# Performance work log

Measured on AMD Instinct MI355X. Metric: run time of the kernel, lower is better.

The kernel has to match this reference:

```python
import jax, jax.numpy as jnp
import numpy as np

N, E = 50000, 800000
IN_DIM, OUT_DIM, REL_DIM = 128, 64, 32
NEG_SLOPE = 0.01  # torch F.leaky_relu default


def setup_inputs() -> dict:
    key = jax.random.key(0)
    ks = jax.random.split(key, 12)
    return {
        "h": jax.random.normal(ks[0], (N, IN_DIM), jnp.float32),
        "relation": jax.random.normal(ks[1], (E, REL_DIM), jnp.float32),
        "score": jax.random.normal(ks[2], (E, 1), jnp.float32),
        "timestamp": jax.random.normal(ks[3], (E, 1), jnp.float32),
        "src": jax.random.randint(ks[4], (E,), 0, N, jnp.int32),
        "dst": jax.random.randint(ks[5], (E,), 0, N, jnp.int32),
        "W_n": jax.random.normal(ks[6], (IN_DIM, OUT_DIM), jnp.float32) / np.sqrt(IN_DIM),
        "W_r": jax.random.normal(ks[7], (REL_DIM, OUT_DIM), jnp.float32) / np.sqrt(REL_DIM),
        "W_s": jax.random.normal(ks[8], (1, OUT_DIM), jnp.float32),
        "W_t": jax.random.normal(ks[9], (1, OUT_DIM), jnp.float32),
        "a": jax.random.normal(ks[10], (5 * OUT_DIM,), jnp.float32) / np.sqrt(5 * OUT_DIM),
    }


def reference(h, relation, score, timestamp, src, dst, W_n, W_r, W_s, W_t, a):
    D = W_n.shape[1]
    z = h @ W_n                     # (N, D)
    er = relation @ W_r             # (E, D)
    es = score @ W_s                # (E, D)
    et = timestamp @ W_t            # (E, D)
    z_src = z[src]                  # (E, D) gather
    z_dst = z[dst]                  # (E, D) gather
    # attn_fc on concat([z_src, z_dst, er, es, et]) == sum of slice dot-products
    a1, a2, a3, a4, a5 = (a[0:D], a[D:2*D], a[2*D:3*D], a[3*D:4*D], a[4*D:5*D])
    logit = z_src @ a1 + z_dst @ a2 + er @ a3 + es @ a4 + et @ a5  # (E,)
    logit = jnp.where(logit >= 0, logit, NEG_SLOPE * logit)        # leaky_relu
    # segment softmax over edges grouped by dst node
    n = z.shape[0]
    seg_max = jax.ops.segment_max(logit, dst, num_segments=n)     # (N,)
    ex = jnp.exp(logit - seg_max[dst])                             # (E,)
    seg_sum = jax.ops.segment_sum(ex, dst, num_segments=n)        # (N,)
    alpha = ex / seg_sum[dst]                                      # (E,)
    # weighted scatter-sum of source features to dst nodes
    h_out = jax.ops.segment_sum(alpha[:, None] * z_src, dst, num_segments=n)  # (N, D)
    return h_out
```

## Files before the change

### kernel.cpp

```cpp
#include <hip/hip_runtime.h>

#define IN_DIM 128
#define OUT_DIM 64
#define REL_DIM 32
#define NEG_SLOPE 0.01f
#define CAP 64

__global__ void k_consts(const float* __restrict__ W_r, const float* __restrict__ W_s,
                         const float* __restrict__ W_t, const float* __restrict__ a,
                         float* __restrict__ consts ) {
    int t = threadIdx.x;
    if (t < REL_DIM) {
        const float* a3 = a + 2 * OUT_DIM;
        float acc = 0.f;
        for (int d = 0; d < OUT_DIM; ++d) acc += W_r[t * OUT_DIM + d] * a3[d];
        consts[t] = acc;
    } else if (t == 32) {
        float acc = 0.f;
        for (int d = 0; d < OUT_DIM; ++d) acc += W_s[d] * a[3 * OUT_DIM + d];
        consts[32] = acc;
    } else if (t == 33) {
        float acc = 0.f;
        for (int d = 0; d < OUT_DIM; ++d) acc += W_t[d] * a[4 * OUT_DIM + d];
        consts[33] = acc;
    }
}

__global__ __launch_bounds__(256) void k_node(const float* __restrict__ h,
                                              const float* __restrict__ W_n,
                                              const float* __restrict__ a,
                                              float* __restrict__ z,
                                              float* __restrict__ s1,
                                              float* __restrict__ s2, int n) {
    __shared__ float hs[IN_DIM * 65];
    __shared__ float s1p[4][64], s2p[4][64];
    int base = blockIdx.x * 64;

    for (int i = threadIdx.x; i < 64 * 32; i += 256) {
        int r = i >> 5;
        int c4 = i & 31;
        float4 v = make_float4(0.f, 0.f, 0.f, 0.f);
        if (base + r < n) v = ((const float4*)(h + (size_t)(base + r) * IN_DIM))[c4];
        int k0 = c4 * 4;
        hs[(k0 + 0) * 65 + r] = v.x;
        hs[(k0 + 1) * 65 + r] = v.y;
        hs[(k0 + 2) * 65 + r] = v.z;
        hs[(k0 + 3) * 65 + r] = v.w;
    }
    __syncthreads();

    int lane = threadIdx.x & 63;
    int w = __builtin_amdgcn_readfirstlane(threadIdx.x >> 6);
    int c0 = w * 16;
    int row = base + lane;

    float acc[16];
    #pragma unroll
    for (int j = 0; j < 16; ++j) acc[j] = 0.f;

    const float* __restrict__ Wslice = W_n + c0;
    #pragma unroll 4
    for (int k = 0; k < IN_DIM; ++k) {
        float hv = hs[k * 65 + lane];
        const float* __restrict__ Wr = Wslice + k * OUT_DIM;
        #pragma unroll
        for (int j = 0; j < 16; ++j) acc[j] = fmaf(hv, Wr[j], acc[j]);
    }

    float p1 = 0.f, p2 = 0.f;
    #pragma unroll
    for (int j = 0; j < 16; ++j) {
        p1 = fmaf(acc[j], a[c0 + j], p1);
        p2 = fmaf(acc[j], a[OUT_DIM + c0 + j], p2);
    }
    s1p[w][lane] = p1;
    s2p[w][lane] = p2;

    if (row < n) {
        float4* zp = (float4*)(z + (size_t)row * OUT_DIM + c0);
        zp[0] = make_float4(acc[0], acc[1], acc[2], acc[3]);
        zp[1] = make_float4(acc[4], acc[5], acc[6], acc[7]);
        zp[2] = make_float4(acc[8], acc[9], acc[10], acc[11]);
        zp[3] = make_float4(acc[12], acc[13], acc[14], acc[15]);
    }
    __syncthreads();
    if (threadIdx.x < 64 && base + (int)threadIdx.x < n) {
        int l = threadIdx.x;
        s1[base + l] = s1p[0][l] + s1p[1][l] + s1p[2][l] + s1p[3][l];
        s2[base + l] = s2p[0][l] + s2p[1][l] + s2p[2][l] + s2p[3][l];
    }
}

__global__ __launch_bounds__(256) void k_fill(const float* __restrict__ rel,
                                              const float* __restrict__ score,
                                              const float* __restrict__ ts,
                                              const int* __restrict__ src,
                                              const int* __restrict__ dst,
                                              const float* __restrict__ s1,
                                              const float* __restrict__ s2,
                                              const float* __restrict__ consts,
                                              int* __restrict__ cnt,
                                              int2* __restrict__ pedge, int E) {
    int tid = blockIdx.x * 256 + threadIdx.x;
    int e = tid >> 3;
    int sub = tid & 7;
    if (e >= E) return;

    float4 w = ((const float4*)consts)[sub];
    float4 v = ((const float4*)rel)[(size_t)e * 8 + sub];
    float dot = v.x * w.x + v.y * w.y + v.z * w.z + v.w * w.w;
    dot += __shfl_xor(dot, 1, 8);
    dot += __shfl_xor(dot, 2, 8);
    dot += __shfl_xor(dot, 4, 8);

    if (sub == 0) {
        int s = src[e], d = dst[e];
        float lg = dot + s1[s] + s2[d] + score[e] * consts[32] + ts[e] * consts[33];
        lg = (lg >= 0.f) ? lg : NEG_SLOPE * lg;
        int rank = atomicAdd(cnt + d, 1);
        if (rank < CAP)
            pedge[((size_t)d << 6) + rank] = make_int2(s, __float_as_int(lg));
    }
}

__global__ __launch_bounds__(256) void k_out(const int* __restrict__ cnt,
                                             const int2* __restrict__ pedge,
                                             const float* __restrict__ z,
                                             float* __restrict__ out, int n) {
    int lane = threadIdx.x & 63;
    int wave = (blockIdx.x * blockDim.x + threadIdx.x) >> 6;
    int nwaves = (gridDim.x * blockDim.x) >> 6;
    int eg = lane >> 4;
    int dl = lane & 15;
    for (int node = wave; node < n; node += nwaves) {
        int deg = min(cnt[node], CAP);
        float4 acc = make_float4(0.f, 0.f, 0.f, 0.f);
        if (deg > 0) {
            int2 pe = make_int2(0, (int)0xff800000u);
            if (lane < deg) pe = pedge[((size_t)node << 6) + lane];
            float v = __int_as_float(pe.y);
            float m = v;
            #pragma unroll
            for (int o = 32; o > 0; o >>= 1) m = fmaxf(m, __shfl_xor(m, o, 64));
            float ex = __expf(v - m);
            float ssum = ex;
            #pragma unroll
            for (int o = 32; o > 0; o >>= 1) ssum += __shfl_xor(ssum, o, 64);
            float alpha = ex * (1.0f / ssum);
            for (int j0 = 0; j0 < deg; j0 += 4) {
                int j = j0 + eg;
                int jc = (j < 64) ? j : 63;
                float wj = __shfl(alpha, jc, 64);
                int  sj = __shfl(pe.x, jc, 64);
                if (j < deg) {
                    float4 zv = ((const float4*)(z + (size_t)sj * OUT_DIM))[dl];
                    acc.x = fmaf(wj, zv.x, acc.x);
                    acc.y = fmaf(wj, zv.y, acc.y);
                    acc.z = fmaf(wj, zv.z, acc.z);
                    acc.w = fmaf(wj, zv.w, acc.w);
                }
            }
        }
        #pragma unroll
        for (int o = 16; o <= 32; o <<= 1) {
            acc.x += __shfl_xor(acc.x, o, 64);
            acc.y += __shfl_xor(acc.y, o, 64);
            acc.z += __shfl_xor(acc.z, o, 64);
            acc.w += __shfl_xor(acc.w, o, 64);
        }
        if (eg == 0) ((float4*)(out + (size_t)node * OUT_DIM))[dl] = acc;
    }
}

extern "C" void kernel_launch(void* const* d_in, const int* in_sizes, int n_in,
                              void* d_out, int out_size, void* d_ws, size_t ws_size,
                              hipStream_t stream) {
    const float* h         = (const float*)d_in[0];
    const float* relation  = (const float*)d_in[1];
    const float* score     = (const float*)d_in[2];
    const float* timestamp = (const float*)d_in[3];
    const int*   src       = (const int*)d_in[4];
    const int*   dst       = (const int*)d_in[5];
    const float* W_n       = (const float*)d_in[6];
    const float* W_r       = (const float*)d_in[7];
    const float* W_s       = (const float*)d_in[8];
    const float* W_t       = (const float*)d_in[9];
    const float* a         = (const float*)d_in[10];

    int n = in_sizes[0] / IN_DIM;
    int E = in_sizes[4];

    float* ws      = (float*)d_ws;
    float* z       = ws;
    float* s1      = z + (size_t)n * OUT_DIM;
    float* s2      = s1 + n;
    float* consts  = s2 + n;
    int*   cnt     = (int*)(consts + 64);
    int2*  pedge   = (int2*)(cnt + n);

    float* out = (float*)d_out;

    hipMemsetAsync(cnt, 0, (size_t)n * sizeof(int), stream);

    k_consts<<<1, 64, 0, stream>>>(W_r, W_s, W_t, a, consts);
    k_node<<<(n + 63) / 64, 256, 0, stream>>>(h, W_n, a, z, s1, s2, n);
    int nfb = (int)(((long long)E * 8 + 255) / 256);
    k_fill<<<nfb, 256, 0, stream>>>(relation, score, timestamp, src, dst,
                                    s1, s2, consts, cnt, pedge, E);
    k_out<<<(n + 3) / 4, 256, 0, stream>>>(cnt, pedge, z, out, n);
}
```

Baseline: 282.0 us.

## Fold memset and constants into kernels, stage W_n in LDS, pair nodes in k_out

The separate memset and k_consts launches are removed. Counter zeroing moves into k_node, and every k_fill block recomputes the relation, score and timestamp attention constants into shared memory. k_node now stages W_n in LDS in two halves instead of reading it from global memory inside the inner loop. k_out handles two destination nodes per wave to expose more independent gathers. The trade-offs are redundant constant computation in every k_fill block, an extra barrier there, and higher LDS use in k_node, which may lower occupancy.

```diff
diff --git a/kernel.cpp b/kernel.cpp
--- a/kernel.cpp
+++ b/kernel.cpp
@@ -6,35 +6,20 @@
 #define NEG_SLOPE 0.01f
 #define CAP 64
 
-__global__ void k_consts(const float* __restrict__ W_r, const float* __restrict__ W_s,
-                         const float* __restrict__ W_t, const float* __restrict__ a,
-                         float* __restrict__ consts ) {
-    int t = threadIdx.x;
-    if (t < REL_DIM) {
-        const float* a3 = a + 2 * OUT_DIM;
-        float acc = 0.f;
-        for (int d = 0; d < OUT_DIM; ++d) acc += W_r[t * OUT_DIM + d] * a3[d];
-        consts[t] = acc;
-    } else if (t == 32) {
-        float acc = 0.f;
-        for (int d = 0; d < OUT_DIM; ++d) acc += W_s[d] * a[3 * OUT_DIM + d];
-        consts[32] = acc;
-    } else if (t == 33) {
-        float acc = 0.f;
-        for (int d = 0; d < OUT_DIM; ++d) acc += W_t[d] * a[4 * OUT_DIM + d];
-        consts[33] = acc;
-    }
-}
-
 __global__ __launch_bounds__(256) void k_node(const float* __restrict__ h,
                                               const float* __restrict__ W_n,
                                               const float* __restrict__ a,
                                               float* __restrict__ z,
                                               float* __restrict__ s1,
-                                              float* __restrict__ s2, int n) {
+                                              float* __restrict__ s2,
+                                              int* __restrict__ cnt, int n) {
     __shared__ float hs[IN_DIM * 65];
+    __shared__ float Wl[64 * OUT_DIM];
     __shared__ float s1p[4][64], s2p[4][64];
     int base = blockIdx.x * 64;
+
+    int gi = blockIdx.x * 256 + threadIdx.x;
+    if (gi < n) cnt[gi] = 0;
 
     for (int i = threadIdx.x; i < 64 * 32; i += 256) {
         int r = i >> 5;
@@ -47,7 +32,6 @@
         hs[(k0 + 2) * 65 + r] = v.z;
         hs[(k0 + 3) * 65 + r] = v.w;
     }
-    __syncthreads();
 
     int lane = threadIdx.x & 63;
     int w = __builtin_amdgcn_readfirstlane(threadIdx.x >> 6);
@@ -58,13 +42,33 @@
     #pragma unroll
     for (int j = 0; j < 16; ++j) acc[j] = 0.f;
 
-    const float* __restrict__ Wslice = W_n + c0;
-    #pragma unroll 4
-    for (int k = 0; k < IN_DIM; ++k) {
-        float hv = hs[k * 65 + lane];
-        const float* __restrict__ Wr = Wslice + k * OUT_DIM;
-        #pragma unroll
-        for (int j = 0; j < 16; ++j) acc[j] = fmaf(hv, Wr[j], acc[j]);
+    for (int kh = 0; kh < 2; ++kh) {
+        __syncthreads();
+        for (int i = threadIdx.x; i < 64 * OUT_DIM / 4; i += 256)
+            ((float4*)Wl)[i] = ((const float4*)(W_n + (size_t)kh * 64 * OUT_DIM))[i];
+        __syncthreads();
+        #pragma unroll 4
+        for (int kk = 0; kk < 64; ++kk) {
+            float hv = hs[(kh * 64 + kk) * 65 + lane];
+            const float4* Wk = (const float4*)(Wl + kk * OUT_DIM + c0);
+            float4 w0 = Wk[0], w1 = Wk[1], w2 = Wk[2], w3 = Wk[3];
+            acc[0]  = fmaf(hv, w0.x, acc[0]);
+            acc[1]  = fmaf(hv, w0.y, acc[1]);
+            acc[2]  = fmaf(hv, w0.z, acc[2]);
+            acc[3]  = fmaf(hv, w0.w, acc[3]);
+            acc[4]  = fmaf(hv, w1.x, acc[4]);
+            acc[5]  = fmaf(hv, w1.y, acc[5]);
+            acc[6]  = fmaf(hv, w1.z, acc[6]);
+            acc[7]  = fmaf(hv, w1.w, acc[7]);
+            acc[8]  = fmaf(hv, w2.x, acc[8]);
+            acc[9]  = fmaf(hv, w2.y, acc[9]);
+            acc[10] = fmaf(hv, w2.z, acc[10]);
+            acc[11] = fmaf(hv, w2.w, acc[11]);
+            acc[12] = fmaf(hv, w3.x, acc[12]);
+            acc[13] = fmaf(hv, w3.y, acc[13]);
+            acc[14] = fmaf(hv, w3.z, acc[14]);
+            acc[15] = fmaf(hv, w3.w, acc[15]);
+        }
     }
 
     float p1 = 0.f, p2 = 0.f;
@@ -98,24 +102,47 @@
                                               const int* __restrict__ dst,
                                               const float* __restrict__ s1,
                                               const float* __restrict__ s2,
-                                              const float* __restrict__ consts,
+                                              const float* __restrict__ W_r,
+                                              const float* __restrict__ W_s,
+                                              const float* __restrict__ W_t,
+                                              const float* __restrict__ a,
                                               int* __restrict__ cnt,
                                               int2* __restrict__ pedge, int E) {
-    int tid = blockIdx.x * 256 + threadIdx.x;
+    __shared__ __align__(16) float cw[36];
+    int t = threadIdx.x;
+    if (t < REL_DIM) {
+        const float* a3 = a + 2 * OUT_DIM;
+        float acc = 0.f;
+        #pragma unroll
+        for (int d2 = 0; d2 < OUT_DIM; ++d2)
+            acc = fmaf(W_r[t * OUT_DIM + d2], a3[d2], acc);
+        cw[t] = acc;
+    } else if (t == 32) {
+        float acc = 0.f;
+        for (int d2 = 0; d2 < OUT_DIM; ++d2) acc = fmaf(W_s[d2], a[3 * OUT_DIM + d2], acc);
+        cw[32] = acc;
+    } else if (t == 33) {
+        float acc = 0.f;
+        for (int d2 = 0; d2 < OUT_DIM; ++d2) acc = fmaf(W_t[d2], a[4 * OUT_DIM + d2], acc);
+        cw[33] = acc;
+    }
+    __syncthreads();
+
+    int tid = blockIdx.x * 256 + t;
     int e = tid >> 3;
     int sub = tid & 7;
     if (e >= E) return;
 
-    float4 w = ((const float4*)consts)[sub];
+    float4 w4 = ((const float4*)cw)[sub];
     float4 v = ((const float4*)rel)[(size_t)e * 8 + sub];
-    float dot = v.x * w.x + v.y * w.y + v.z * w.z + v.w * w.w;
+    float dot = v.x * w4.x + v.y * w4.y + v.z * w4.z + v.w * w4.w;
     dot += __shfl_xor(dot, 1, 8);
     dot += __shfl_xor(dot, 2, 8);
     dot += __shfl_xor(dot, 4, 8);
 
     if (sub == 0) {
         int s = src[e], d = dst[e];
-        float lg = dot + s1[s] + s2[d] + score[e] * consts[32] + ts[e] * consts[33];
+        float lg = dot + s1[s] + s2[d] + score[e] * cw[32] + ts[e] * cw[33];
         lg = (lg >= 0.f) ? lg : NEG_SLOPE * lg;
         int rank = atomicAdd(cnt + d, 1);
         if (rank < CAP)
@@ -132,43 +159,73 @@
     int nwaves = (gridDim.x * blockDim.x) >> 6;
     int eg = lane >> 4;
     int dl = lane & 15;
-    for (int node = wave; node < n; node += nwaves) {
-        int deg = min(cnt[node], CAP);
-        float4 acc = make_float4(0.f, 0.f, 0.f, 0.f);
-        if (deg > 0) {
-            int2 pe = make_int2(0, (int)0xff800000u);
-            if (lane < deg) pe = pedge[((size_t)node << 6) + lane];
-            float v = __int_as_float(pe.y);
-            float m = v;
-            #pragma unroll
-            for (int o = 32; o > 0; o >>= 1) m = fmaxf(m, __shfl_xor(m, o, 64));
-            float ex = __expf(v - m);
-            float ssum = ex;
-            #pragma unroll
-            for (int o = 32; o > 0; o >>= 1) ssum += __shfl_xor(ssum, o, 64);
-            float alpha = ex * (1.0f / ssum);
-            for (int j0 = 0; j0 < deg; j0 += 4) {
-                int j = j0 + eg;
-                int jc = (j < 64) ? j : 63;
-                float wj = __shfl(alpha, jc, 64);
-                int  sj = __shfl(pe.x, jc, 64);
-                if (j < deg) {
-                    float4 zv = ((const float4*)(z + (size_t)sj * OUT_DIM))[dl];
-                    acc.x = fmaf(wj, zv.x, acc.x);
-                    acc.y = fmaf(wj, zv.y, acc.y);
-                    acc.z = fmaf(wj, zv.z, acc.z);
-                    acc.w = fmaf(wj, zv.w, acc.w);
-                }
+    int npairs = (n + 1) >> 1;
+    for (int p = wave; p < npairs; p += nwaves) {
+        int nA = p * 2, nB = p * 2 + 1;
+        int degA = min(cnt[nA], CAP);
+        int degB = (nB < n) ? min(cnt[nB], CAP) : 0;
+        int2 peA = make_int2(0, (int)0xff800000u);
+        int2 peB = make_int2(0, (int)0xff800000u);
+        if (lane < degA) peA = pedge[((size_t)nA << 6) + lane];
+        if (lane < degB) peB = pedge[((size_t)nB << 6) + lane];
+        float vA = __int_as_float(peA.y), vB = __int_as_float(peB.y);
+        float mA = vA, mB = vB;
+        #pragma unroll
+        for (int o = 32; o > 0; o >>= 1) {
+            mA = fmaxf(mA, __shfl_xor(mA, o, 64));
+            mB = fmaxf(mB, __shfl_xor(mB, o, 64));
+        }
+        float exA = __expf(vA - mA);
+        float exB = __expf(vB - mB);
+        float sA = exA, sB = exB;
+        #pragma unroll
+        for (int o = 32; o > 0; o >>= 1) {
+            sA += __shfl_xor(sA, o, 64);
+            sB += __shfl_xor(sB, o, 64);
+        }
+        float alA = exA * (1.0f / sA);
+        float alB = exB * (1.0f / sB);
+        float4 accA = make_float4(0.f, 0.f, 0.f, 0.f);
+        float4 accB = make_float4(0.f, 0.f, 0.f, 0.f);
+        int jmax = max(degA, degB);
+        for (int j0 = 0; j0 < jmax; j0 += 4) {
+            int j = j0 + eg;
+            int jc = (j < 64) ? j : 63;
+            float wA = __shfl(alA, jc, 64);
+            int  sjA = __shfl(peA.x, jc, 64);
+            float wB = __shfl(alB, jc, 64);
+            int  sjB = __shfl(peB.x, jc, 64);
+            if (j < degA) {
+                float4 zv = ((const float4*)(z + (size_t)sjA * OUT_DIM))[dl];
+                accA.x = fmaf(wA, zv.x, accA.x);
+                accA.y = fmaf(wA, zv.y, accA.y);
+                accA.z = fmaf(wA, zv.z, accA.z);
+                accA.w = fmaf(wA, zv.w, accA.w);
             }
+            if (j < degB) {
+                float4 zv = ((const float4*)(z + (size_t)sjB * OUT_DIM))[dl];
+                accB.x = fmaf(wB, zv.x, accB.x);
+                accB.y = fmaf(wB, zv.y, accB.y);
+                accB.z = fmaf(wB, zv.z, accB.z);
+                accB.w = fmaf(wB, zv.w, accB.w);
+            }
         }
         #pragma unroll
         for (int o = 16; o <= 32; o <<= 1) {
-            acc.x += __shfl_xor(acc.x, o, 64);
-            acc.y += __shfl_xor(acc.y, o, 64);
-            acc.z += __shfl_xor(acc.z, o, 64);
-            acc.w += __shfl_xor(acc.w, o, 64);
-        }
-        if (eg == 0) ((float4*)(out + (size_t)node * OUT_DIM))[dl] = acc;
+            accA.x += __shfl_xor(accA.x, o, 64);
+            accA.y += __shfl_xor(accA.y, o, 64);
+            accA.z += __shfl_xor(accA.z, o, 64);
+            accA.w += __shfl_xor(accA.w, o, 64);
+            accB.x += __shfl_xor(accB.x, o, 64);
+            accB.y += __shfl_xor(accB.y, o, 64);
+            accB.z += __shfl_xor(accB.z, o, 64);
+            accB.w += __shfl_xor(accB.w, o, 64);
+        }
+        if (eg == 0) {
+            ((float4*)(out + (size_t)nA * OUT_DIM))[dl] = accA;
+        } else if (eg == 1 && nB < n) {
+            ((float4*)(out + (size_t)nB * OUT_DIM))[dl] = accB;
+        }
     }
 }
 
@@ -190,22 +247,21 @@
     int n = in_sizes[0] / IN_DIM;
     int E = in_sizes[4];
 
-    float* ws      = (float*)d_ws;
-    float* z       = ws;
-    float* s1      = z + (size_t)n * OUT_DIM;
-    float* s2      = s1 + n;
-    float* consts  = s2 + n;
-    int*   cnt     = (int*)(consts + 64);
-    int2*  pedge   = (int2*)(cnt + n);
+    float* ws   = (float*)d_ws;
+    float* z    = ws;
+    float* s1   = z + (size_t)n * OUT_DIM;
+    float* s2   = s1 + n;
+    int*   cnt  = (int*)(s2 + n);
+    int2*  pedge = (int2*)(cnt + n);
 
     float* out = (float*)d_out;
 
-    hipMemsetAsync(cnt, 0, (size_t)n * sizeof(int), stream);
-
-    k_consts<<<1, 64, 0, stream>>>(W_r, W_s, W_t, a, consts);
-    k_node<<<(n + 63) / 64, 256, 0, stream>>>(h, W_n, a, z, s1, s2, n);
+    k_node<<<(n + 63) / 64, 256, 0, stream>>>(h, W_n, a, z, s1, s2, cnt, n);
+
     int nfb = (int)(((long long)E * 8 + 255) / 256);
     k_fill<<<nfb, 256, 0, stream>>>(relation, score, timestamp, src, dst,
-                                    s1, s2, consts, cnt, pedge, E);
-    k_out<<<(n + 3) / 4, 256, 0, stream>>>(cnt, pedge, z, out, n);
-}
+                                    s1, s2, W_r, W_s, W_t, a, cnt, pedge, E);
+
+    int npairs = (n + 1) >> 1;
+    k_out<<<(npairs + 3) / 4, 256, 0, stream>>>(cnt, pedge, z, out, n);
+}
```

Result: slower. 312.6 us (+10.8%).
